# Kernel optimization log

Hardware: AMD Instinct MI355X
Metric: run time of the kernel (lower is better)

The kernel has to match this reference:

```python
import jax, jax.numpy as jnp
import numpy as np

B, S, D_IN, D_OUT = 4, 2048, 1024, 1024


def setup_inputs() -> dict:
    key = jax.random.key(0)
    k1, k2, k3, k4 = jax.random.split(key, 4)
    scale = 1.0 / np.sqrt(D_IN)
    return {
        "x": jax.random.normal(k1, (B, S, D_IN), dtype=jnp.float32),
        "W_q": jax.random.normal(k2, (D_IN, D_OUT), dtype=jnp.float32) * scale,
        "W_k": jax.random.normal(k3, (D_IN, D_OUT), dtype=jnp.float32) * scale,
        "W_v": jax.random.normal(k4, (D_IN, D_OUT), dtype=jnp.float32) * scale,
    }


def reference(x, W_q, W_k, W_v):
    # x: [B, S, D_IN]; weights stored as [D_IN, D_OUT] (transpose of torch Linear)
    q = x @ W_q  # [B, S, D_OUT]
    k = x @ W_k
    v = x @ W_v
    inv_sqrt_d = 1.0 / jnp.sqrt(jnp.asarray(k.shape[-1], dtype=q.dtype))
    scores = jnp.einsum("bqd,bkd->bqk", q, k) * inv_sqrt_d  # [B, S, S]
    n = x.shape[1]
    causal_mask = jnp.triu(jnp.ones((n, n), dtype=bool), k=1)  # True above diagonal
    scores = jnp.where(causal_mask, -jnp.inf, scores)
    attn = jax.nn.softmax(scores, axis=-1)  # dropout p=0.0 -> identity
    return jnp.einsum("bqk,bkd->bqd", attn, v)  # [B, S, D_OUT]
```

## Files before the change

### kernel.cpp

```cpp
#include <hip/hip_runtime.h>
#include <hip/hip_bf16.h>
#include <stdint.h>

typedef __bf16 bf16;
typedef bf16 bf16x8 __attribute__((ext_vector_type(8)));
typedef float f32x4 __attribute__((ext_vector_type(4)));

#define NB   4
#define SS   2048
#define DI   1024
#define DOUT 1024

__device__ __forceinline__ void gload_lds16(const void* g, void* l) {
  __builtin_amdgcn_global_load_lds(
      (const __attribute__((address_space(1))) void*)g,
      (__attribute__((address_space(3))) void*)l, 16, 0, 0);
}

#define BARX  { __builtin_amdgcn_s_barrier(); __builtin_amdgcn_sched_barrier(0); }
#define VMW12 asm volatile("s_waitcnt vmcnt(12)" ::: "memory")
#define VMW8  asm volatile("s_waitcnt vmcnt(8)"  ::: "memory")
#define VMW6  asm volatile("s_waitcnt vmcnt(6)"  ::: "memory")
#define VMW4  asm volatile("s_waitcnt vmcnt(4)"  ::: "memory")
#define VMW3  asm volatile("s_waitcnt vmcnt(3)"  ::: "memory")
#define VMW0  asm volatile("s_waitcnt vmcnt(0)"  ::: "memory")

__device__ __forceinline__ bf16x8 cvt8(float4 a, float4 b) {
  bf16x8 v;
  v[0] = (bf16)a.x; v[1] = (bf16)a.y; v[2] = (bf16)a.z; v[3] = (bf16)a.w;
  v[4] = (bf16)b.x; v[5] = (bf16)b.y; v[6] = (bf16)b.z; v[7] = (bf16)b.w;
  return v;
}

__device__ __forceinline__ void r5_loop3(
    const bf16* __restrict__ Ag, int lda,
    const bf16* __restrict__ Bg, int ldb,
    int nt, char* lds, f32x4 (&acc)[8][4])
{
  const int tid = threadIdx.x, lane = tid & 63, w = tid >> 6;
  const int g    = (tid & 3) ^ ((tid >> 3) & 3);
  const int srow = tid >> 2;
  const int l15  = lane & 15, lg = lane >> 4;
  const int aoff = l15 * 64 + ((lg ^ ((l15 >> 1) & 3)) << 4);

  auto STG = [&](int t, int p) {
    char* Ab = lds + p * 24576;
    char* Bb = lds + p * 24576 + 8192;
#pragma unroll
    for (int i = 0; i < 2; ++i)
      gload_lds16(Ag + (size_t)(i * 64 + srow) * lda + t * 32 + g * 8,
                  Ab + i * 4096 + tid * 16);
#pragma unroll
    for (int i = 0; i < 4; ++i)
      gload_lds16(Bg + (size_t)(i * 64 + srow) * ldb + t * 32 + g * 8,
                  Bb + i * 4096 + tid * 16);
  };

  auto CMP = [&](int p) {
    const char* Ab = lds + p * 24576;
    const char* Bb = lds + p * 24576 + 8192 + w * 4096;
    bf16x8 a[8], bq[4];
#pragma unroll
    for (int am = 0; am < 8; ++am) a[am] = *(const bf16x8*)(Ab + am * 1024 + aoff);
#pragma unroll
    for (int fn = 0; fn < 4; ++fn) bq[fn] = *(const bf16x8*)(Bb + fn * 1024 + aoff);
    __builtin_amdgcn_s_setprio(1);
#pragma unroll
    for (int am = 0; am < 8; ++am)
#pragma unroll
      for (int fn = 0; fn < 4; ++fn)
        acc[am][fn] = __builtin_amdgcn_mfma_f32_16x16x32_bf16(
            a[am], bq[fn], acc[am][fn], 0, 0, 0);
    __builtin_amdgcn_s_setprio(0);
  };

  STG(0, 0);
  STG(1, 1);
  int pw = 2, pr = 0;
  for (int t = 0; t < nt - 2; ++t) {
    STG(t + 2, pw);
    VMW12;
    BARX;
    CMP(pr);
    BARX;
    pw = (pw == 2) ? 0 : pw + 1;
    pr = (pr == 2) ? 0 : pr + 1;
  }
  VMW6; BARX; CMP(pr); BARX;
  pr = (pr == 2) ? 0 : pr + 1;
  VMW0; BARX; CMP(pr);
}

__device__ __forceinline__ void r5h_loop3(
    const bf16* __restrict__ Ag, int lda,
    const bf16* __restrict__ Bg, int ldb,
    int nt, char* lds, f32x4 (&acc)[4][4])
{
  const int tid = threadIdx.x, lane = tid & 63, wid = tid >> 6;
  const int wr = wid >> 1, wc = wid & 1;
  const int g    = (tid & 3) ^ ((tid >> 3) & 3);
  const int srow = tid >> 2;
  const int l15  = lane & 15, lg = lane >> 4;
  const int aoff = l15 * 64 + ((lg ^ ((l15 >> 1) & 3)) << 4);

  auto STG = [&](int t, int p) {
    char* Ab = lds + p * 16384;
    char* Bb = lds + p * 16384 + 8192;
#pragma unroll
    for (int i = 0; i < 2; ++i) {
      gload_lds16(Ag + (size_t)(i * 64 + srow) * lda + t * 32 + g * 8,
                  Ab + i * 4096 + tid * 16);
      gload_lds16(Bg + (size_t)(i * 64 + srow) * ldb + t * 32 + g * 8,
                  Bb + i * 4096 + tid * 16);
    }
  };

  auto CMP = [&](int p) {
    const char* Ab = lds + p * 16384 + wr * 4096;
    const char* Bb = lds + p * 16384 + 8192 + wc * 4096;
    bf16x8 a[4], bq[4];
#pragma unroll
    for (int fm = 0; fm < 4; ++fm) a[fm] = *(const bf16x8*)(Ab + fm * 1024 + aoff);
#pragma unroll
    for (int fn = 0; fn < 4; ++fn) bq[fn] = *(const bf16x8*)(Bb + fn * 1024 + aoff);
    __builtin_amdgcn_s_setprio(1);
#pragma unroll
    for (int fm = 0; fm < 4; ++fm)
#pragma unroll
      for (int fn = 0; fn < 4; ++fn)
        acc[fm][fn] = __builtin_amdgcn_mfma_f32_16x16x32_bf16(
            a[fm], bq[fn], acc[fm][fn], 0, 0, 0);
    __builtin_amdgcn_s_setprio(0);
  };

  STG(0, 0);
  STG(1, 1);
  int pw = 2, pr = 0;
  for (int t = 0; t < nt - 2; ++t) {
    STG(t + 2, pw);
    VMW8;
    BARX;
    CMP(pr);
    BARX;
    pw = (pw == 2) ? 0 : pw + 1;
    pr = (pr == 2) ? 0 : pr + 1;
  }
  VMW4; BARX; CMP(pr); BARX;
  pr = (pr == 2) ? 0 : pr + 1;
  VMW0; BARX; CMP(pr);
}

__device__ __forceinline__ void r5q_loop3(
    const bf16* __restrict__ Ag, int lda,
    const bf16* __restrict__ Bg, int ldb,
    int nt, char* lds, f32x4 (&acc)[4][2])
{
  const int tid = threadIdx.x, lane = tid & 63, wid = tid >> 6;
  const int wr = wid >> 1, wc = wid & 1;
  const int g    = (tid & 3) ^ ((tid >> 3) & 3);
  const int srow = tid >> 2;
  const int l15  = lane & 15, lg = lane >> 4;
  const int aoff = l15 * 64 + ((lg ^ ((l15 >> 1) & 3)) << 4);

  auto STG = [&](int t, int p) {
    char* Ab = lds + p * 12288;
    char* Bb = lds + p * 12288 + 8192;
#pragma unroll
    for (int i = 0; i < 2; ++i)
      gload_lds16(Ag + (size_t)(i * 64 + srow) * lda + t * 32 + g * 8,
                  Ab + i * 4096 + tid * 16);
    gload_lds16(Bg + (size_t)srow * ldb + t * 32 + g * 8, Bb + tid * 16);
  };

  auto CMP = [&](int p) {
    const char* Ab = lds + p * 12288 + wr * 4096;
    const char* Bb = lds + p * 12288 + 8192 + wc * 2048;
    bf16x8 a[4], bq[2];
#pragma unroll
    for (int fm = 0; fm < 4; ++fm) a[fm] = *(const bf16x8*)(Ab + fm * 1024 + aoff);
#pragma unroll
    for (int fn = 0; fn < 2; ++fn) bq[fn] = *(const bf16x8*)(Bb + fn * 1024 + aoff);
    __builtin_amdgcn_s_setprio(1);
#pragma unroll
    for (int fm = 0; fm < 4; ++fm)
#pragma unroll
      for (int fn = 0; fn < 2; ++fn)
        acc[fm][fn] = __builtin_amdgcn_mfma_f32_16x16x32_bf16(
            a[fm], bq[fn], acc[fm][fn], 0, 0, 0);
    __builtin_amdgcn_s_setprio(0);
  };

  STG(0, 0);
  STG(1, 1);
  int pw = 2, pr = 0;
  for (int t = 0; t < nt - 2; ++t) {
    STG(t + 2, pw);
    VMW6;
    BARX;
    CMP(pr);
    BARX;
    pw = (pw == 2) ? 0 : pw + 1;
    pr = (pr == 2) ? 0 : pr + 1;
  }
  VMW3; BARX; CMP(pr); BARX;
  pr = (pr == 2) ? 0 : pr + 1;
  VMW0; BARX; CMP(pr);
}

__device__ __forceinline__ void acc_zero4(f32x4 (&acc)[4][4]) {
#pragma unroll
  for (int i = 0; i < 4; ++i)
#pragma unroll
    for (int j = 0; j < 4; ++j)
      acc[i][j] = (f32x4){0.f, 0.f, 0.f, 0.f};
}

__global__ __launch_bounds__(256) void k_prep(const float* __restrict__ x,
                                              bf16* __restrict__ xb,
                                              const float* __restrict__ Wq,
                                              const float* __restrict__ Wk,
                                              const float* __restrict__ Wv,
                                              bf16* __restrict__ WTv,
                                              float* __restrict__ MTp,
                                              float* __restrict__ RS) {
  __shared__ __align__(16) char lds[16384];
  const int bid = blockIdx.x;
  const int tid = threadIdx.x;

  if (bid < 256) {
    const int tile = bid >> 2, s = bid & 3;
    const int m0 = (tile >> 3) * 128, n0 = (tile & 7) * 128;
    const int k0 = s * 256;
    const int lane = tid & 63, wid = tid >> 6;
    const int wr = wid >> 1, wc = wid & 1;
    const int g    = (tid & 3) ^ ((tid >> 3) & 3);
    const int srow = tid >> 2;
    const int l15  = lane & 15, lg = lane >> 4;
    const int aoff = l15 * 64 + ((lg ^ ((l15 >> 1) & 3)) << 4);

    const float* ap0 = Wk + (size_t)(m0 + srow) * DI + k0 + g * 8;
    const float* ap1 = Wk + (size_t)(m0 + 64 + srow) * DI + k0 + g * 8;
    const float* bp0 = Wq + (size_t)(n0 + srow) * DI + k0 + g * 8;
    const float* bp1 = Wq + (size_t)(n0 + 64 + srow) * DI + k0 + g * 8;

    f32x4 acc[4][4];
    acc_zero4(acc);

    float4 A00 = *(const float4*)(ap0), A01 = *(const float4*)(ap0 + 4);
    float4 A10 = *(const float4*)(ap1), A11 = *(const float4*)(ap1 + 4);
    float4 B00 = *(const float4*)(bp0), B01 = *(const float4*)(bp0 + 4);
    float4 B10 = *(const float4*)(bp1), B11 = *(const float4*)(bp1 + 4);

    for (int t = 0; t < 8; ++t) {
      float4 nA00, nA01, nA10, nA11, nB00, nB01, nB10, nB11;
      if (t < 7) {
        const int o = (t + 1) * 32;
        nA00 = *(const float4*)(ap0 + o); nA01 = *(const float4*)(ap0 + o + 4);
        nA10 = *(const float4*)(ap1 + o); nA11 = *(const float4*)(ap1 + o + 4);
        nB00 = *(const float4*)(bp0 + o); nB01 = *(const float4*)(bp0 + o + 4);
        nB10 = *(const float4*)(bp1 + o); nB11 = *(const float4*)(bp1 + o + 4);
      }
      *(bf16x8*)(lds + tid * 16)         = cvt8(A00, A01);
      *(bf16x8*)(lds + 4096 + tid * 16)  = cvt8(A10, A11);
      *(bf16x8*)(lds + 8192 + tid * 16)  = cvt8(B00, B01);
      *(bf16x8*)(lds + 12288 + tid * 16) = cvt8(B10, B11);
      __syncthreads();
      {
        const char* Ab = lds + wr * 4096;
        const char* Bb = lds + 8192 + wc * 4096;
        bf16x8 a[4], bq[4];
#pragma unroll
        for (int fm = 0; fm < 4; ++fm) a[fm] = *(const bf16x8*)(Ab + fm * 1024 + aoff);
#pragma unroll
        for (int fn = 0; fn < 4; ++fn) bq[fn] = *(const bf16x8*)(Bb + fn * 1024 + aoff);
#pragma unroll
        for (int fm = 0; fm < 4; ++fm)
#pragma unroll
          for (int fn = 0; fn < 4; ++fn)
            acc[fm][fn] = __builtin_amdgcn_mfma_f32_16x16x32_bf16(
                a[fm], bq[fn], acc[fm][fn], 0, 0, 0);
      }
      __syncthreads();
      A00 = nA00; A01 = nA01; A10 = nA10; A11 = nA11;
      B00 = nB00; B01 = nB01; B10 = nB10; B11 = nB11;
    }

    float* MPs = MTp + (size_t)s * (1024 * 1024);
    const int r4 = (lane >> 4) * 4, cn = lane & 15;
#pragma unroll
    for (int fm = 0; fm < 4; ++fm)
#pragma unroll
      for (int fn = 0; fn < 4; ++fn) {
        const int rowb = m0 + wr * 64 + fm * 16 + r4;
        const int col  = n0 + wc * 64 + fn * 16 + cn;
#pragma unroll
        for (int rr = 0; rr < 4; ++rr)
          MPs[(size_t)(rowb + rr) * 1024 + col] = acc[fm][fn][rr];
      }
  } else if (bid < 4352) {
    const size_t i = ((size_t)(bid - 256) * 256 + tid) * 8;
    const float4 a = *(const float4*)(x + i);
    const float4 c = *(const float4*)(x + i + 4);
    *(bf16x8*)(xb + i) = cvt8(a, c);
  } else if (bid < 5376) {
    float (*t)[33] = (float (*)[33])lds;
    const int tt = bid - 4352;
    const int c0 = (tt & 31) * 32, k0 = (tt >> 5) * 32;
    const int tx = tid & 31, ty = tid >> 5;
#pragma unroll
    for (int i = 0; i < 4; ++i)
      t[ty + 8 * i][tx] = Wv[(size_t)(k0 + ty + 8 * i) * DI + c0 + tx];
    __syncthreads();
#pragma unroll
    for (int i = 0; i < 4; ++i)
      WTv[(size_t)(c0 + ty + 8 * i) * DI + k0 + tx] = (bf16)t[tx][ty + 8 * i];
  } else {
    float4 z = {0.f, 0.f, 0.f, 0.f};
#pragma unroll
    for (int i = 0; i < 8; ++i)
      *(float4*)(RS + (size_t)tid * 32 + i * 4) = z;
  }
}

__global__ __launch_bounds__(256) void k_mtred(const float* __restrict__ MTp,
                                               bf16* __restrict__ MT) {
  const size_t i = ((size_t)blockIdx.x * 256 + threadIdx.x) * 8;
  float4 a = *(const float4*)(MTp + i);
  float4 b = *(const float4*)(MTp + i + 4);
#pragma unroll
  for (int s = 1; s < 4; ++s) {
    const float* p = MTp + (size_t)s * (1024 * 1024) + i;
    const float4 c = *(const float4*)p;
    const float4 d = *(const float4*)(p + 4);
    a.x += c.x; a.y += c.y; a.z += c.z; a.w += c.w;
    b.x += d.x; b.y += d.y; b.z += d.z; b.w += d.w;
  }
  *(bf16x8*)(MT + i) = cvt8(a, b);
}

__global__ __launch_bounds__(256, 2) void k_tv(const bf16* __restrict__ X,
                                               const bf16* __restrict__ MT,
                                               const bf16* __restrict__ WTv,
                                               bf16* __restrict__ T,
                                               bf16* __restrict__ VT) {
  __shared__ __align__(16) char lds[73728];
  const int bid  = blockIdx.x;
  const int wgid = (bid & 7) * 64 + (bid >> 3);
  const int m0 = (wgid >> 3) * 128;
  const int n0 = (wgid & 7) * 256;

  const bf16* Bg = (n0 < 1024) ? MT + (size_t)n0 * 1024
                               : WTv + (size_t)(n0 - 1024) * 1024;

  f32x4 acc[8][4];
#pragma unroll
  for (int i = 0; i < 8; ++i)
#pragma unroll
    for (int j = 0; j < 4; ++j)
      acc[i][j] = (f32x4){0.f, 0.f, 0.f, 0.f};

  r5_loop3(X + (size_t)m0 * 1024, 1024, Bg, 1024, 32, lds, acc);

  const int lane = threadIdx.x & 63, w = threadIdx.x >> 6;
  const int r4 = (lane >> 4) * 4;
  const int cn = lane & 15;
  if (n0 < 1024) {
#pragma unroll
    for (int am = 0; am < 8; ++am) {
      const int row = m0 + am * 16 + r4;
#pragma unroll
      for (int fn = 0; fn < 4; ++fn) {
        const int n = n0 + w * 64 + fn * 16 + cn;
        const size_t base = (size_t)row * 1024 + n;
#pragma unroll
        for (int r = 0; r < 4; ++r)
          T[base + (size_t)r * 1024] = (bf16)acc[am][fn][r];
      }
    }
  } else {
    const int b_ = m0 >> 11;
    const int sb = m0 & 2047;
#pragma unroll
    for (int am = 0; am < 8; ++am)
#pragma unroll
      for (int fn = 0; fn < 4; ++fn) {
        const int d  = (n0 - 1024) + w * 64 + fn * 16 + cn;
        const int s0 = sb + am * 16 + r4;
        ushort4 pk;
        pk.x = __builtin_bit_cast(unsigned short, (bf16)acc[am][fn][0]);
        pk.y = __builtin_bit_cast(unsigned short, (bf16)acc[am][fn][1]);
        pk.z = __builtin_bit_cast(unsigned short, (bf16)acc[am][fn][2]);
        pk.w = __builtin_bit_cast(unsigned short, (bf16)acc[am][fn][3]);
        *(ushort4*)(VT + ((size_t)b_ * DOUT + d) * SS + s0) = pk;
      }
  }
}

__global__ __launch_bounds__(256, 3) void k_gemm_qk(const bf16* __restrict__ T,
                                                    const bf16* __restrict__ XB,
                                                    bf16* __restrict__ E,
                                                    float* __restrict__ RS) {
  __shared__ __align__(16) char lds[49152];
  const int c  = blockIdx.x & 7;
  const int li = blockIdx.x >> 3;
  const bool full = (li < 64);
  const int gt = full ? (c * 68 + li) : (c * 68 + 64 + ((li - 64) >> 1));
  const int nh = full ? 0 : ((li - 64) & 1);

  const int b = gt / 136;
  int r = gt % 136;
  int i = 0;
  for (;;) { const int cnt = i + 1; if (r < cnt) break; r -= cnt; ++i; }
  const int m0 = i * 128;

  bf16* Eb = E + (size_t)b * SS * SS;
  float* RSb = RS + (size_t)b * SS;
  const float scale = 0.03125f;
  const int lane = threadIdx.x & 63, wid = threadIdx.x >> 6;
  const int wr = wid >> 1, wc = wid & 1;
  const int r4 = (lane >> 4) * 4, cn = lane & 15;

  float rsum[4][4];
#pragma unroll
  for (int fm = 0; fm < 4; ++fm)
#pragma unroll
    for (int rr = 0; rr < 4; ++rr) rsum[fm][rr] = 0.f;

  if (full) {
    const int n0 = r * 128;
    f32x4 acc[4][4];
    acc_zero4(acc);
    r5h_loop3(T  + ((size_t)b * SS + m0) * 1024, 1024,
              XB + ((size_t)b * SS + n0) * 1024, 1024, 32, lds, acc);
#pragma unroll
    for (int fm = 0; fm < 4; ++fm)
#pragma unroll
      for (int fn = 0; fn < 4; ++fn) {
        const int n = n0 + wc * 64 + fn * 16 + cn;
        const int rowb = m0 + wr * 64 + fm * 16 + r4;
        const size_t bofs = (size_t)rowb * SS + n;
#pragma unroll
        for (int rr = 0; rr < 4; ++rr) {
          const float e = (n <= rowb + rr) ? __expf(acc[fm][fn][rr] * scale) : 0.f;
          Eb[bofs + (size_t)rr * SS] = (bf16)e;
          rsum[fm][rr] += e;
        }
      }
  } else {
    const int n0 = r * 128 + nh * 64;
    f32x4 acc[4][2];
#pragma unroll
    for (int ii = 0; ii < 4; ++ii)
#pragma unroll
      for (int jj = 0; jj < 2; ++jj)
        acc[ii][jj] = (f32x4){0.f, 0.f, 0.f, 0.f};
    r5q_loop3(T  + ((size_t)b * SS + m0) * 1024, 1024,
              XB + ((size_t)b * SS + n0) * 1024, 1024, 32, lds, acc);
#pragma unroll
    for (int fm = 0; fm < 4; ++fm)
#pragma unroll
      for (int fn = 0; fn < 2; ++fn) {
        const int n = n0 + wc * 32 + fn * 16 + cn;
        const int rowb = m0 + wr * 64 + fm * 16 + r4;
        const size_t bofs = (size_t)rowb * SS + n;
#pragma unroll
        for (int rr = 0; rr < 4; ++rr) {
          const float e = (n <= rowb + rr) ? __expf(acc[fm][fn][rr] * scale) : 0.f;
          Eb[bofs + (size_t)rr * SS] = (bf16)e;
          rsum[fm][rr] += e;
        }
      }
  }

#pragma unroll
  for (int fm = 0; fm < 4; ++fm)
#pragma unroll
    for (int rr = 0; rr < 4; ++rr) {
      float s = rsum[fm][rr];
      s += __shfl_xor(s, 1);
      s += __shfl_xor(s, 2);
      s += __shfl_xor(s, 4);
      s += __shfl_xor(s, 8);
      if (cn == 0)
        atomicAdd(&RSb[m0 + wr * 64 + fm * 16 + r4 + rr], s);
    }
}

__global__ __launch_bounds__(256, 3) void k_gemm_pv(const bf16* __restrict__ P,
                                                    const bf16* __restrict__ VT,
                                                    const float* __restrict__ RS,
                                                    float* __restrict__ Out) {
  __shared__ __align__(16) char lds[49152];
  const int wfl = blockIdx.x;
  const int h = wfl >> 8;
  const int r = wfl & 255;
  const int b = r >> 6;
  const int t = r & 63;
  const int ip = t >> 3;
  const int j = t & 7;
  const int i = h ? (15 - ip) : ip;
  const int m0 = i * 128, n0 = j * 128;
  const int nt = 4 * (i + 1);

  f32x4 acc[4][4];
  acc_zero4(acc);
  r5h_loop3(P  + (size_t)b * SS * SS   + (size_t)m0 * SS, SS,
            VT + (size_t)b * DOUT * SS + (size_t)n0 * SS, SS,
            nt, lds, acc);

  float* Ob = Out + (size_t)b * SS * DOUT;
  const float* RSb = RS + (size_t)b * SS;
  const int lane = threadIdx.x & 63, wid = threadIdx.x >> 6;
  const int wr = wid >> 1, wc = wid & 1;
  const int r4 = (lane >> 4) * 4, cn = lane & 15;
#pragma unroll
  for (int fm = 0; fm < 4; ++fm) {
    const int rowb = m0 + wr * 64 + fm * 16 + r4;
    const float4 rs4 = *(const float4*)(RSb + rowb);
    float inv[4];
    inv[0] = 1.0f / rs4.x; inv[1] = 1.0f / rs4.y;
    inv[2] = 1.0f / rs4.z; inv[3] = 1.0f / rs4.w;
#pragma unroll
    for (int fn = 0; fn < 4; ++fn) {
      const int n = n0 + wc * 64 + fn * 16 + cn;
      const size_t bofs = (size_t)rowb * DOUT + n;
#pragma unroll
      for (int rr = 0; rr < 4; ++rr)
        Ob[bofs + (size_t)rr * DOUT] = acc[fm][fn][rr] * inv[rr];
    }
  }
}

extern "C" void kernel_launch(void* const* d_in, const int* in_sizes, int n_in,
                              void* d_out, int out_size, void* d_ws, size_t ws_size,
                              hipStream_t stream) {
  const float* x  = (const float*)d_in[0];
  const float* Wq = (const float*)d_in[1];
  const float* Wk = (const float*)d_in[2];
  const float* Wv = (const float*)d_in[3];
  float* out = (float*)d_out;
  char* ws = (char*)d_ws;

  bf16*  T   = (bf16*)(ws);
  bf16*  VT  = (bf16*)(ws + ((size_t)16 << 20));
  bf16*  E   = (bf16*)(ws + ((size_t)32 << 20));
  float* MTp = (float*)(ws + ((size_t)32 << 20));
  bf16*  XB  = (bf16*)(ws + ((size_t)64 << 20));
  bf16*  WTv = (bf16*)(ws + ((size_t)80 << 20));
  bf16*  MT  = (bf16*)(ws + ((size_t)82 << 20));
  float* RS  = (float*)(ws + ((size_t)84 << 20));

  k_prep<<<5377, 256, 0, stream>>>(x, XB, Wq, Wk, Wv, WTv, MTp, RS);
  k_mtred<<<512, 256, 0, stream>>>(MTp, MT);
  k_tv<<<512, 256, 0, stream>>>(XB, MT, WTv, T, VT);
  k_gemm_qk<<<576, 256, 0, stream>>>(T, XB, E, RS);
  k_gemm_pv<<<512, 256, 0, stream>>>(E, VT, RS, out);
}
```

Before: 124.7 us.

## Rewrite k_tv as 256x256 tile, 8-wave GEMM with interleaved half-tile prefetch

Replaces the 128x256 triple-buffered k_tv GEMM with a 256x256 tile per 512-thread block using a 2x4 wave grid and 64-wide k steps. LDS is double buffered and the global-to-LDS loads for the next tiles are issued in quarters between four MFMA quadrant phases, separated by barriers. The goal is more reuse per loaded byte and better overlap of memory traffic with MFMA work. The 128 KB LDS footprint limits occupancy, and the grid is halved to 256 blocks.

```diff
diff --git a/kernel.cpp b/kernel.cpp
--- a/kernel.cpp
+++ b/kernel.cpp
@@ -30,65 +30,6 @@
   v[0] = (bf16)a.x; v[1] = (bf16)a.y; v[2] = (bf16)a.z; v[3] = (bf16)a.w;
   v[4] = (bf16)b.x; v[5] = (bf16)b.y; v[6] = (bf16)b.z; v[7] = (bf16)b.w;
   return v;
-}
-
-__device__ __forceinline__ void r5_loop3(
-    const bf16* __restrict__ Ag, int lda,
-    const bf16* __restrict__ Bg, int ldb,
-    int nt, char* lds, f32x4 (&acc)[8][4])
-{
-  const int tid = threadIdx.x, lane = tid & 63, w = tid >> 6;
-  const int g    = (tid & 3) ^ ((tid >> 3) & 3);
-  const int srow = tid >> 2;
-  const int l15  = lane & 15, lg = lane >> 4;
-  const int aoff = l15 * 64 + ((lg ^ ((l15 >> 1) & 3)) << 4);
-
-  auto STG = [&](int t, int p) {
-    char* Ab = lds + p * 24576;
-    char* Bb = lds + p * 24576 + 8192;
-#pragma unroll
-    for (int i = 0; i < 2; ++i)
-      gload_lds16(Ag + (size_t)(i * 64 + srow) * lda + t * 32 + g * 8,
-                  Ab + i * 4096 + tid * 16);
-#pragma unroll
-    for (int i = 0; i < 4; ++i)
-      gload_lds16(Bg + (size_t)(i * 64 + srow) * ldb + t * 32 + g * 8,
-                  Bb + i * 4096 + tid * 16);
-  };
-
-  auto CMP = [&](int p) {
-    const char* Ab = lds + p * 24576;
-    const char* Bb = lds + p * 24576 + 8192 + w * 4096;
-    bf16x8 a[8], bq[4];
-#pragma unroll
-    for (int am = 0; am < 8; ++am) a[am] = *(const bf16x8*)(Ab + am * 1024 + aoff);
-#pragma unroll
-    for (int fn = 0; fn < 4; ++fn) bq[fn] = *(const bf16x8*)(Bb + fn * 1024 + aoff);
-    __builtin_amdgcn_s_setprio(1);
-#pragma unroll
-    for (int am = 0; am < 8; ++am)
-#pragma unroll
-      for (int fn = 0; fn < 4; ++fn)
-        acc[am][fn] = __builtin_amdgcn_mfma_f32_16x16x32_bf16(
-            a[am], bq[fn], acc[am][fn], 0, 0, 0);
-    __builtin_amdgcn_s_setprio(0);
-  };
-
-  STG(0, 0);
-  STG(1, 1);
-  int pw = 2, pr = 0;
-  for (int t = 0; t < nt - 2; ++t) {
-    STG(t + 2, pw);
-    VMW12;
-    BARX;
-    CMP(pr);
-    BARX;
-    pw = (pw == 2) ? 0 : pw + 1;
-    pr = (pr == 2) ? 0 : pr + 1;
-  }
-  VMW6; BARX; CMP(pr); BARX;
-  pr = (pr == 2) ? 0 : pr + 1;
-  VMW0; BARX; CMP(pr);
 }
 
 __device__ __forceinline__ void r5h_loop3(
@@ -338,20 +279,40 @@
   *(bf16x8*)(MT + i) = cvt8(a, b);
 }
 
-__global__ __launch_bounds__(256, 2) void k_tv(const bf16* __restrict__ X,
+__global__ __launch_bounds__(512, 2) void k_tv(const bf16* __restrict__ X,
                                                const bf16* __restrict__ MT,
                                                const bf16* __restrict__ WTv,
                                                bf16* __restrict__ T,
                                                bf16* __restrict__ VT) {
-  __shared__ __align__(16) char lds[73728];
+  __shared__ __align__(16) char lds[131072];
   const int bid  = blockIdx.x;
-  const int wgid = (bid & 7) * 64 + (bid >> 3);
-  const int m0 = (wgid >> 3) * 128;
+  const int wgid = (bid & 7) * 32 + (bid >> 3);
+  const int m0 = (wgid >> 3) * 256;
   const int n0 = (wgid & 7) * 256;
 
+  const bf16* Ag = X + (size_t)m0 * 1024;
   const bf16* Bg = (n0 < 1024) ? MT + (size_t)n0 * 1024
                                : WTv + (size_t)(n0 - 1024) * 1024;
 
+  const int tid = threadIdx.x, lane = tid & 63, w = tid >> 6;
+  const int wr = w >> 2, wcn = w & 3;
+  const int l15 = lane & 15, lg = lane >> 4;
+  const int srow8 = tid >> 3, kq = tid & 7;
+
+  const int aBase = wr * 16384 + l15 * 128 + lg * 16;
+  const int bBase = wcn * 8192 + l15 * 128 + lg * 16;
+
+  auto STGH = [&](int t, int q) {
+    char* dst = lds + (t & 1) * 65536 + ((q & 2) ? 32768 : 0)
+                + ((q & 1) ? 16384 : 0);
+    const bf16* src = (q & 2) ? Bg : Ag;
+    const int rb = (q & 1) ? 128 : 0;
+#pragma unroll
+    for (int j = 0; j < 2; ++j)
+      gload_lds16(src + (size_t)(rb + j * 64 + srow8) * 1024 + t * 64 + kq * 8,
+                  dst + j * 8192 + tid * 16);
+  };
+
   f32x4 acc[8][4];
 #pragma unroll
   for (int i = 0; i < 8; ++i)
@@ -359,40 +320,125 @@
     for (int j = 0; j < 4; ++j)
       acc[i][j] = (f32x4){0.f, 0.f, 0.f, 0.f};
 
-  r5_loop3(X + (size_t)m0 * 1024, 1024, Bg, 1024, 32, lds, acc);
-
-  const int lane = threadIdx.x & 63, w = threadIdx.x >> 6;
+  STGH(0, 0); STGH(0, 1); STGH(0, 2); STGH(0, 3);
+  STGH(1, 0); STGH(1, 1); STGH(1, 2);
+
+  for (int t = 0; t < 16; ++t) {
+    if (t < 15) { VMW6; } else { VMW0; }
+    BARX;
+    const char* Ab = lds + (t & 1) * 65536;
+    const char* Bb = Ab + 32768;
+    bf16x8 a[8], b[4], b2[4];
+
+#pragma unroll
+    for (int fm = 0; fm < 4; ++fm)
+#pragma unroll
+      for (int kk = 0; kk < 2; ++kk)
+        a[fm * 2 + kk] = *(const bf16x8*)(Ab + aBase + fm * 2048 + kk * 64);
+#pragma unroll
+    for (int fn = 0; fn < 2; ++fn)
+#pragma unroll
+      for (int kk = 0; kk < 2; ++kk)
+        b[fn * 2 + kk] = *(const bf16x8*)(Bb + bBase + fn * 2048 + kk * 64);
+    if (t + 1 < 16) STGH(t + 1, 3);
+    BARX;
+    __builtin_amdgcn_s_setprio(1);
+#pragma unroll
+    for (int fm = 0; fm < 4; ++fm)
+#pragma unroll
+      for (int fn = 0; fn < 2; ++fn)
+#pragma unroll
+        for (int kk = 0; kk < 2; ++kk)
+          acc[fm][fn] = __builtin_amdgcn_mfma_f32_16x16x32_bf16(
+              a[fm * 2 + kk], b[fn * 2 + kk], acc[fm][fn], 0, 0, 0);
+    __builtin_amdgcn_s_setprio(0);
+    BARX;
+
+#pragma unroll
+    for (int fn = 0; fn < 2; ++fn)
+#pragma unroll
+      for (int kk = 0; kk < 2; ++kk)
+        b2[fn * 2 + kk] = *(const bf16x8*)(Bb + bBase + 4096 + fn * 2048 + kk * 64);
+    BARX;
+    __builtin_amdgcn_s_setprio(1);
+#pragma unroll
+    for (int fm = 0; fm < 4; ++fm)
+#pragma unroll
+      for (int fn = 0; fn < 2; ++fn)
+#pragma unroll
+        for (int kk = 0; kk < 2; ++kk)
+          acc[fm][2 + fn] = __builtin_amdgcn_mfma_f32_16x16x32_bf16(
+              a[fm * 2 + kk], b2[fn * 2 + kk], acc[fm][2 + fn], 0, 0, 0);
+    __builtin_amdgcn_s_setprio(0);
+    BARX;
+
+#pragma unroll
+    for (int fm = 0; fm < 4; ++fm)
+#pragma unroll
+      for (int kk = 0; kk < 2; ++kk)
+        a[fm * 2 + kk] = *(const bf16x8*)(Ab + aBase + 8192 + fm * 2048 + kk * 64);
+    if (t + 2 < 16) STGH(t + 2, 2);
+    BARX;
+    __builtin_amdgcn_s_setprio(1);
+#pragma unroll
+    for (int fm = 0; fm < 4; ++fm)
+#pragma unroll
+      for (int fn = 0; fn < 2; ++fn)
+#pragma unroll
+        for (int kk = 0; kk < 2; ++kk)
+          acc[4 + fm][fn] = __builtin_amdgcn_mfma_f32_16x16x32_bf16(
+              a[fm * 2 + kk], b[fn * 2 + kk], acc[4 + fm][fn], 0, 0, 0);
+    __builtin_amdgcn_s_setprio(0);
+    BARX;
+
+    if (t + 2 < 16) { STGH(t + 2, 0); STGH(t + 2, 1); }
+    BARX;
+    __builtin_amdgcn_s_setprio(1);
+#pragma unroll
+    for (int fm = 0; fm < 4; ++fm)
+#pragma unroll
+      for (int fn = 0; fn < 2; ++fn)
+#pragma unroll
+        for (int kk = 0; kk < 2; ++kk)
+          acc[4 + fm][2 + fn] = __builtin_amdgcn_mfma_f32_16x16x32_bf16(
+              a[fm * 2 + kk], b2[fn * 2 + kk], acc[4 + fm][2 + fn], 0, 0, 0);
+    __builtin_amdgcn_s_setprio(0);
+    BARX;
+  }
+
   const int r4 = (lane >> 4) * 4;
   const int cn = lane & 15;
   if (n0 < 1024) {
 #pragma unroll
-    for (int am = 0; am < 8; ++am) {
-      const int row = m0 + am * 16 + r4;
+    for (int fm = 0; fm < 8; ++fm) {
+      const int row = m0 + wr * 128 + fm * 16 + r4;
 #pragma unroll
       for (int fn = 0; fn < 4; ++fn) {
-        const int n = n0 + w * 64 + fn * 16 + cn;
+        const int n = n0 + wcn * 64 + fn * 16 + cn;
         const size_t base = (size_t)row * 1024 + n;
 #pragma unroll
         for (int r = 0; r < 4; ++r)
-          T[base + (size_t)r * 1024] = (bf16)acc[am][fn][r];
+          T[base + (size_t)r * 1024] = (bf16)acc[fm][fn][r];
       }
     }
   } else {
     const int b_ = m0 >> 11;
-    const int sb = m0 & 2047;
-#pragma unroll
-    for (int am = 0; am < 8; ++am)
-#pragma unroll
-      for (int fn = 0; fn < 4; ++fn) {
-        const int d  = (n0 - 1024) + w * 64 + fn * 16 + cn;
-        const int s0 = sb + am * 16 + r4;
+    const int sb = (m0 & 2047) + wr * 128 + r4;
+#pragma unroll
+    for (int fn = 0; fn < 4; ++fn) {
+      const int d = (n0 - 1024) + wcn * 64 + fn * 16 + cn;
+      bf16* vp = VT + ((size_t)b_ * DOUT + d) * SS;
+#pragma unroll
+      for (int fm = 0; fm < 8; ++fm) {
+        const int s0 = sb + fm * 16;
         ushort4 pk;
-        pk.x = __builtin_bit_cast(unsigned short, (bf16)acc[am][fn][0]);
-        pk.y = __builtin_bit_cast(unsigned short, (bf16)acc[am][fn][1]);
-        pk.z = __builtin_bit_cast(unsigned short, (bf16)acc[am][fn][2]);
-        pk.w = __builtin_bit_cast(unsigned short, (bf16)acc[am][fn][3]);
-        *(ushort4*)(VT + ((size_t)b_ * DOUT + d) * SS + s0) = pk;
+        pk.x = __builtin_bit_cast(unsigned short, (bf16)acc[fm][fn][0]);
+        pk.y = __builtin_bit_cast(unsigned short, (bf16)acc[fm][fn][1]);
+        pk.z = __builtin_bit_cast(unsigned short, (bf16)acc[fm][fn][2]);
+        pk.w = __builtin_bit_cast(unsigned short, (bf16)acc[fm][fn][3]);
+        *(ushort4*)(vp + s0) = pk;
       }
+    }
   }
 }
 
@@ -552,7 +598,7 @@
 
   k_prep<<<5377, 256, 0, stream>>>(x, XB, Wq, Wk, Wv, WTv, MTp, RS);
   k_mtred<<<512, 256, 0, stream>>>(MTp, MT);
-  k_tv<<<512, 256, 0, stream>>>(XB, MT, WTv, T, VT);
+  k_tv<<<256, 512, 0, stream>>>(XB, MT, WTv, T, VT);
   k_gemm_qk<<<576, 256, 0, stream>>>(T, XB, E, RS);
   k_gemm_pv<<<512, 256, 0, stream>>>(E, VT, RS, out);
 }
```

Result: slower. 132.5 us (+6.2%).
